# Kernel tuning notes

Hardware: AMD Instinct MI355X
Metric: run time of the kernel (lower is better)

## Reference

```python
import jax, jax.numpy as jnp
import numpy as np

NTYPES = 8
EXCLUDE = [(0, 1), (2, 3)]
NF, NLOC, NNEI = 4, 16384, 128
NALL = 32768


def _build_type_mask(ntypes, exclude):
    ex = set()
    for a, b in exclude:
        ex.add((a, b))
        ex.add((b, a))
    tm = np.ones((ntypes + 1, ntypes + 1), dtype=np.float32)
    for ti, tj in ex:
        tm[tj, ti] = 0.0
    return tm.reshape(-1)  # flattened [(ntypes+1)^2]


def setup_inputs() -> dict:
    key = jax.random.key(0)
    k1, k2 = jax.random.split(key)
    # nlist in [-1, NALL): -1 marks a missing neighbor
    nlist = jax.random.randint(k1, (NF, NLOC, NNEI), -1, NALL, dtype=jnp.int32)
    atype_ext = jax.random.randint(k2, (NF, NALL), 0, NTYPES, dtype=jnp.int32)
    type_mask = jnp.asarray(_build_type_mask(NTYPES, EXCLUDE))
    return {"nlist": nlist, "atype_ext": atype_ext, "type_mask": type_mask, "ntypes": NTYPES}


def reference(nlist, atype_ext, type_mask, ntypes):
    nf, nloc, nnei = nlist.shape
    nall = atype_ext.shape[1]
    # append virtual type `ntypes` used for -1 (padding) neighbors
    ae = jnp.concatenate(
        [atype_ext, jnp.full((nf, 1), ntypes, dtype=atype_ext.dtype)], axis=-1
    )  # [nf, nall+1]
    type_i = atype_ext[:, :nloc] * (ntypes + 1)  # [nf, nloc]
    index = jnp.where(nlist == -1, nall, nlist)  # [nf, nloc, nnei]
    type_j = jnp.take_along_axis(ae, index.reshape(nf, nloc * nnei), axis=1)
    type_j = type_j.reshape(nf, nloc, nnei)
    type_ij = type_i[:, :, None] + type_j  # flat index into type_mask table
    mask = type_mask[type_ij]  # [nf, nloc, nnei]
    return mask
```

## Files before the change

kernel.cpp:

```cpp
#include <hip/hip_runtime.h>

#define NF    4
#define NLOC  16384
#define NNEI  128
#define NALL  32768
#define TMASK_N 81

__global__ void __launch_bounds__(256) pair_exclude_mask_kernel(
    const int* __restrict__ nlist,
    const int* __restrict__ atype_ext,
    const float* __restrict__ type_mask,
    const int* __restrict__ ntypes_p,
    float* __restrict__ out)
{
    __shared__ float smask[TMASK_N];
    if (threadIdx.x < TMASK_N) smask[threadIdx.x] = type_mask[threadIdx.x];
    __syncthreads();

    const int ntypes = ntypes_p[0];

    const long long total4 = (long long)NF * NLOC * NNEI / 4;
    long long g = (long long)blockIdx.x * blockDim.x + threadIdx.x;
    if (g >= total4) return;

    const long long e = g * 4;
    const int f  = (int)(e / ((long long)NLOC * NNEI));
    const int r  = (int)(e - (long long)f * NLOC * NNEI);
    const int i  = r / NNEI;

    const int ti = atype_ext[f * NALL + i] * (ntypes + 1);

    const int4 nl = *reinterpret_cast<const int4*>(nlist + e);
    const int* ae = atype_ext + (long long)f * NALL;

    float4 m;
    {
        int tj = (nl.x == -1) ? ntypes : ae[nl.x];
        m.x = smask[ti + tj];
    }
    {
        int tj = (nl.y == -1) ? ntypes : ae[nl.y];
        m.y = smask[ti + tj];
    }
    {
        int tj = (nl.z == -1) ? ntypes : ae[nl.z];
        m.z = smask[ti + tj];
    }
    {
        int tj = (nl.w == -1) ? ntypes : ae[nl.w];
        m.w = smask[ti + tj];
    }

    *reinterpret_cast<float4*>(out + e) = m;
}

extern "C" void kernel_launch(void* const* d_in, const int* in_sizes, int n_in,
                              void* d_out, int out_size, void* d_ws, size_t ws_size,
                              hipStream_t stream) {
    const int*   nlist     = (const int*)d_in[0];
    const int*   atype_ext = (const int*)d_in[1];
    const float* type_mask = (const float*)d_in[2];
    const int*   ntypes_p  = (const int*)d_in[3];
    float*       out       = (float*)d_out;

    const long long total4 = (long long)NF * NLOC * NNEI / 4;
    const int block = 256;
    const int grid  = (int)((total4 + block - 1) / block);

    pair_exclude_mask_kernel<<<grid, block, 0, stream>>>(
        nlist, atype_ext, type_mask, ntypes_p, out);
}
```

Baseline: 108.6 us.

## Stage per-frame atom types as bytes in LDS and loop over a frame per block

A pre-pass kernel packs atom types into a byte table in workspace. Each block of the main kernel then copies its frame's 32 KB type table into shared memory, so the random neighbour gathers become LDS reads instead of global loads. Each thread now handles several quads in an unrolled loop across a fixed grid of 256 blocks per frame. This adds a second launch and a per-block 32 KB LDS fill, which limits occupancy.

```diff
diff --git a/kernel.cpp b/kernel.cpp
--- a/kernel.cpp
+++ b/kernel.cpp
@@ -4,54 +4,85 @@
 #define NLOC  16384
 #define NNEI  128
 #define NALL  32768
-#define TMASK_N 81
+#define TMASK_LDS 96
 
-__global__ void __launch_bounds__(256) pair_exclude_mask_kernel(
+#define ELEMS_PER_FRAME (NLOC * NNEI)
+#define Q4_PER_FRAME    (ELEMS_PER_FRAME / 4)
+#define BLOCKS_PER_FRAME 256
+#define THREADS 256
+#define ITERS (Q4_PER_FRAME / (BLOCKS_PER_FRAME * THREADS))
+
+__global__ void __launch_bounds__(256) build_type_table(
+    const int* __restrict__ atype_ext,
+    unsigned char* __restrict__ ttab)
+{
+    const int t = blockIdx.x * blockDim.x + threadIdx.x;
+    const int4 v = reinterpret_cast<const int4*>(atype_ext)[t];
+    uchar4 b;
+    b.x = (unsigned char)v.x;
+    b.y = (unsigned char)v.y;
+    b.z = (unsigned char)v.z;
+    b.w = (unsigned char)v.w;
+    reinterpret_cast<uchar4*>(ttab)[t] = b;
+}
+
+__global__ void __launch_bounds__(THREADS) pair_exclude_mask_kernel(
     const int* __restrict__ nlist,
-    const int* __restrict__ atype_ext,
+    const unsigned char* __restrict__ ttab,
     const float* __restrict__ type_mask,
     const int* __restrict__ ntypes_p,
     float* __restrict__ out)
 {
-    __shared__ float smask[TMASK_N];
-    if (threadIdx.x < TMASK_N) smask[threadIdx.x] = type_mask[threadIdx.x];
+    __shared__ unsigned char stt[NALL];
+    __shared__ float smask[TMASK_LDS];
+
+    const int f = blockIdx.x / BLOCKS_PER_FRAME;
+    const int b = blockIdx.x % BLOCKS_PER_FRAME;
+
+    {
+        const uint4* src = reinterpret_cast<const uint4*>(ttab + (size_t)f * NALL);
+        uint4* dst = reinterpret_cast<uint4*>(stt);
+        #pragma unroll
+        for (int k = 0; k < NALL / 16 / THREADS; ++k)
+            dst[threadIdx.x + k * THREADS] = src[threadIdx.x + k * THREADS];
+        if (threadIdx.x < 81) smask[threadIdx.x] = type_mask[threadIdx.x];
+    }
     __syncthreads();
 
     const int ntypes = ntypes_p[0];
+    const int np1 = ntypes + 1;
 
-    const long long total4 = (long long)NF * NLOC * NNEI / 4;
-    long long g = (long long)blockIdx.x * blockDim.x + threadIdx.x;
-    if (g >= total4) return;
+    const int* nl_base = nlist + (size_t)f * ELEMS_PER_FRAME;
+    float* out_base = out + (size_t)f * ELEMS_PER_FRAME;
+    const int q0 = b * (THREADS * ITERS);
 
-    const long long e = g * 4;
-    const int f  = (int)(e / ((long long)NLOC * NNEI));
-    const int r  = (int)(e - (long long)f * NLOC * NNEI);
-    const int i  = r / NNEI;
+    #pragma unroll
+    for (int it = 0; it < ITERS; ++it) {
+        const int q = q0 + it * THREADS + threadIdx.x;
+        const int4 nl = reinterpret_cast<const int4*>(nl_base)[q];
+        const int e = q * 4;
+        const int i = e >> 7;
+        const int ti = (int)stt[i] * np1;
 
-    const int ti = atype_ext[f * NALL + i] * (ntypes + 1);
-
-    const int4 nl = *reinterpret_cast<const int4*>(nlist + e);
-    const int* ae = atype_ext + (long long)f * NALL;
-
-    float4 m;
-    {
-        int tj = (nl.x == -1) ? ntypes : ae[nl.x];
-        m.x = smask[ti + tj];
+        float4 m;
+        {
+            const int tj = (nl.x == -1) ? ntypes : (int)stt[nl.x];
+            m.x = smask[ti + tj];
+        }
+        {
+            const int tj = (nl.y == -1) ? ntypes : (int)stt[nl.y];
+            m.y = smask[ti + tj];
+        }
+        {
+            const int tj = (nl.z == -1) ? ntypes : (int)stt[nl.z];
+            m.z = smask[ti + tj];
+        }
+        {
+            const int tj = (nl.w == -1) ? ntypes : (int)stt[nl.w];
+            m.w = smask[ti + tj];
+        }
+        reinterpret_cast<float4*>(out_base)[q] = m;
     }
-    {
-        int tj = (nl.y == -1) ? ntypes : ae[nl.y];
-        m.y = smask[ti + tj];
-    }
-    {
-        int tj = (nl.z == -1) ? ntypes : ae[nl.z];
-        m.z = smask[ti + tj];
-    }
-    {
-        int tj = (nl.w == -1) ? ntypes : ae[nl.w];
-        m.w = smask[ti + tj];
-    }
-
-    *reinterpret_cast<float4*>(out + e) = m;
 }
 
 extern "C" void kernel_launch(void* const* d_in, const int* in_sizes, int n_in,
@@ -62,11 +93,10 @@
     const float* type_mask = (const float*)d_in[2];
     const int*   ntypes_p  = (const int*)d_in[3];
     float*       out       = (float*)d_out;
+    unsigned char* ttab    = (unsigned char*)d_ws;
 
-    const long long total4 = (long long)NF * NLOC * NNEI / 4;
-    const int block = 256;
-    const int grid  = (int)((total4 + block - 1) / block);
+    build_type_table<<<(NF * NALL / 4) / 256, 256, 0, stream>>>(atype_ext, ttab);
 
-    pair_exclude_mask_kernel<<<grid, block, 0, stream>>>(
-        nlist, atype_ext, type_mask, ntypes_p, out);
+    pair_exclude_mask_kernel<<<NF * BLOCKS_PER_FRAME, THREADS, 0, stream>>>(
+        nlist, ttab, type_mask, ntypes_p, out);
 }
```

Result: faster. 91.21 us (-16.1%).
